# Performance work log

Measured on AMD Instinct MI355X. Metric: run time of the kernel, lower is better.

The kernel has to match this reference:

```python
import jax, jax.numpy as jnp
import numpy as np

W_, H_, D_ = 45, 30, 13
TEXT = 226
NVID = W_ * H_ * D_            # 17550 video tokens
L = TEXT + NVID                # 17776 total tokens
BLK = 128
NKEEP = 32
NBLK = (L + BLK - 1) // BLK    # 139 blocks
LPAD = NBLK * BLK              # 17792
LEVELS = (1, 2, 4, 8)
MASK_RATIOS = ((1, 0.0, 0.05), (2, 0.05, 0.15), (4, 0.15, 0.25), (8, 0.25, 0.5), (0, 0.5, 1.0))
NEG = -1e30

def _sgn(x):
    return (x > 0) - (x < 0)

def _gen3d(x, y, z, ax, ay, az, bx, by, bz, cx, cy, cz):
    w = abs(ax + ay + az); h = abs(bx + by + bz); d = abs(cx + cy + cz)
    dax, day, daz = _sgn(ax), _sgn(ay), _sgn(az)
    dbx, dby, dbz = _sgn(bx), _sgn(by), _sgn(bz)
    dcx, dcy, dcz = _sgn(cx), _sgn(cy), _sgn(cz)
    if h == 1 and d == 1:
        for _ in range(w):
            yield (x, y, z); x += dax; y += day; z += daz
        return
    if w == 1 and d == 1:
        for _ in range(h):
            yield (x, y, z); x += dbx; y += dby; z += dbz
        return
    if w == 1 and h == 1:
        for _ in range(d):
            yield (x, y, z); x += dcx; y += dcy; z += dcz
        return
    ax2, ay2, az2 = ax // 2, ay // 2, az // 2
    bx2, by2, bz2 = bx // 2, by // 2, bz // 2
    cx2, cy2, cz2 = cx // 2, cy // 2, cz // 2
    w2 = abs(ax2 + ay2 + az2); h2 = abs(bx2 + by2 + bz2); d2 = abs(cx2 + cy2 + cz2)
    if (w2 % 2) and (w > 2): ax2 += dax; ay2 += day; az2 += daz
    if (h2 % 2) and (h > 2): bx2 += dbx; by2 += dby; bz2 += dbz
    if (d2 % 2) and (d > 2): cx2 += dcx; cy2 += dcy; cz2 += dcz
    if (2 * w > 3 * h) and (2 * w > 3 * d):
        yield from _gen3d(x, y, z, ax2, ay2, az2, bx, by, bz, cx, cy, cz)
        yield from _gen3d(x + ax2, y + ay2, z + az2, ax - ax2, ay - ay2, az - az2, bx, by, bz, cx, cy, cz)
    elif 3 * h > 4 * d:
        yield from _gen3d(x, y, z, bx2, by2, bz2, cx, cy, cz, ax2, ay2, az2)
        yield from _gen3d(x + bx2, y + by2, z + bz2, ax, ay, az, bx - bx2, by - by2, bz - bz2, cx, cy, cz)
        yield from _gen3d(x + (ax - dax) + (bx2 - dbx), y + (ay - day) + (by2 - dby), z + (az - daz) + (bz2 - dbz), -bx2, -by2, -bz2, cx, cy, cz, -(ax - ax2), -(ay - ay2), -(az - az2))
    elif 3 * d > 4 * h:
        yield from _gen3d(x, y, z, cx2, cy2, cz2, ax2, ay2, az2, bx, by, bz)
        yield from _gen3d(x + cx2, y + cy2, z + cz2, ax, ay, az, bx, by, bz, cx - cx2, cy - cy2, cz - cz2)
        yield from _gen3d(x + (ax - dax) + (cx2 - dcx), y + (ay - day) + (cy2 - dcy), z + (az - daz) + (cz2 - dcz), -cx2, -cy2, -cz2, -(ax - ax2), -(ay - ay2), -(az - az2), bx, by, bz)
    else:
        yield from _gen3d(x, y, z, bx2, by2, bz2, cx2, cy2, cz2, ax2, ay2, az2)
        yield from _gen3d(x + bx2, y + by2, z + bz2, cx, cy, cz, ax2, ay2, az2, bx - bx2, by - by2, bz - bz2)
        yield from _gen3d(x + (bx2 - dbx) + (cx - dcx), y + (by2 - dby) + (cy - dcy), z + (bz2 - dbz) + (cz - dcz), ax, ay, az, -bx2, -by2, -bz2, -(cx - cx2), -(cy - cy2), -(cz - cz2))
        yield from _gen3d(x + (ax - dax) + bx2 + (cx - dcx), y + (ay - day) + by2 + (cy - dcy), z + (az - daz) + bz2 + (cz - dcz), -cx, -cy, -cz, -(ax - ax2), -(ay - ay2), -(az - az2), bx - bx2, by - by2, bz - bz2)

def _gilbert3d(w, h, d):
    if w >= h and w >= d:
        yield from _gen3d(0, 0, 0, w, 0, 0, 0, h, 0, 0, 0, d)
    elif h >= w and h >= d:
        yield from _gen3d(0, 0, 0, 0, h, 0, w, 0, 0, 0, 0, d)
    else:
        yield from _gen3d(0, 0, 0, 0, 0, d, w, 0, 0, 0, h, 0)

def _perms():
    o2g = np.zeros(NVID, np.int64); g2o = np.zeros(NVID, np.int64)
    for g, (x, y, z) in enumerate(_gilbert3d(W_, H_, D_)):
        c = x + W_ * (y + H_ * z)
        o2g[g] = c; g2o[c] = g
    return jnp.asarray(o2g), jnp.asarray(g2o)

O2G, G2O = _perms()

def _sample(x, key):
    # random_sample_tokens: same NKEEP indices (per b,h) reused for every block
    B, Hh, _, Dd = x.shape
    r = jax.random.uniform(key, (B, Hh, BLK))
    idx = jax.lax.top_k(r, NKEEP)[1]                    # [B,H,NKEEP]
    xb = x.reshape(B, Hh, NBLK, BLK, Dd)
    s = jnp.take_along_axis(xb, idx[:, :, None, :, None], axis=3)
    return s.reshape(B, Hh, NBLK * NKEEP, Dd)

def _make_mask(q, k):
    # torch.no_grad() mask path
    q = jax.lax.stop_gradient(q); k = jax.lax.stop_gradient(k)
    pad = LPAD - L
    qp = jnp.pad(q, ((0, 0), (0, 0), (0, pad), (0, 0)), mode='edge')
    kp = jnp.pad(k, ((0, 0), (0, 0), (0, pad), (0, 0)), mode='edge')
    kq, kk = jax.random.split(jax.random.key(0))
    sq = _sample(qp, kq); sk = _sample(kp, kk)
    scale = 1.0 / float(np.sqrt(q.shape[-1]))
    attn = jax.nn.softmax(jnp.einsum('bhid,bhjd->bhij', sq, sk) * scale, axis=-1)
    B, Hh = attn.shape[:2]
    # sum-pool NKEEP x NKEEP -> block-level pooled attention [B,H,NBLK,NBLK]
    pool = attn.reshape(B, Hh, NBLK, NKEEP, NBLK, NKEEP).sum(axis=(3, 5))
    # rank of each column within its row (descending) == scatter over sorted indices
    rank = jnp.argsort(jnp.argsort(-pool, axis=-1), axis=-1)
    mask = jnp.zeros(pool.shape, jnp.int32)
    for val, s, e in MASK_RATIOS:
        si = max(0, int(NBLK * s)); ei = min(NBLK, int(NBLK * e))
        if si < ei and val != 0:
            mask = jnp.where((rank >= si) & (rank < ei), jnp.int32(val), mask)
    mask = mask.at[:, :, :, -2:].set(1)
    mask = mask.at[:, :, -2:, :].set(1)
    return mask

def _pooled_kv(kp, vp):
    # per-level mean-pooled K/V per key block, padded to BLK slots + log-count bias
    B, Hh, _, Dd = kp.shape
    valid = (jnp.arange(LPAD) < L).astype(kp.dtype).reshape(NBLK, BLK)
    kb = kp.reshape(B, Hh, NBLK, BLK, Dd)
    vb = vp.reshape(B, Hh, NBLK, BLK, Dd)
    Ks, Vs, Bs = [], [], []
    for m in LEVELS:
        g = BLK // m
        cnt = valid.reshape(NBLK, g, m).sum(-1)          # [NBLK,g] valid tokens per group
        den = jnp.maximum(cnt, 1.0)
        kpl = kb.reshape(B, Hh, NBLK, g, m, Dd).sum(4) / den[None, None, :, :, None]
        vpl = vb.reshape(B, Hh, NBLK, g, m, Dd).sum(4) / den[None, None, :, :, None]
        bias = jnp.where(cnt > 0, jnp.log(den), NEG)
        padn = BLK - g
        Ks.append(jnp.pad(kpl, ((0, 0), (0, 0), (0, 0), (0, padn), (0, 0))))
        Vs.append(jnp.pad(vpl, ((0, 0), (0, 0), (0, 0), (0, padn), (0, 0))))
        Bs.append(jnp.pad(bias, ((0, 0), (0, padn)), constant_values=NEG))
    return jnp.stack(Ks, 3), jnp.stack(Vs, 3), jnp.stack(Bs, 1)

def _sparse_attn(q, k, v, mask):
    B, Hh, _, Dd = q.shape
    pad = LPAD - L
    zp = ((0, 0), (0, 0), (0, pad), (0, 0))
    qp = jnp.pad(q, zp); kp = jnp.pad(k, zp); vp = jnp.pad(v, zp)
    KL, VL, BIAS = _pooled_kv(kp, vp)   # [B,H,NBLK,4,BLK,D], bias [NBLK,4,BLK]
    table = np.zeros(9, np.int32)
    table[1], table[2], table[4], table[8] = 0, 1, 2, 3
    lvl = jnp.asarray(table)[mask]
    act = mask > 0
    scale = 1.0 / float(np.sqrt(Dd))
    qb = jnp.transpose(qp.reshape(B, Hh, NBLK, BLK, Dd), (2, 0, 1, 3, 4))
    lvl_t = jnp.transpose(lvl, (2, 0, 1, 3))
    act_t = jnp.transpose(act, (2, 0, 1, 3))
    biasB = jnp.broadcast_to(BIAS[None, None], (B, Hh, NBLK, len(LEVELS), BLK))
    def body(carry, xs):
        qi, li, ai = xs                 # [B,H,BLK,D], [B,H,NBLK], [B,H,NBLK]
        sel = li[:, :, :, None, None]
        Ksel = jnp.take_along_axis(KL, sel[..., None], axis=3)[:, :, :, 0]   # [B,H,NBLK,BLK,D]
        Vsel = jnp.take_along_axis(VL, sel[..., None], axis=3)[:, :, :, 0]
        bsel = jnp.take_along_axis(biasB, sel, axis=3)[:, :, :, 0]           # [B,H,NBLK,BLK]
        logit = jnp.einsum('bhqd,bhknd->bhqkn', qi, Ksel) * scale
        logit = logit + jnp.where(ai[:, :, None, :, None], bsel[:, :, None], NEG)
        p = jax.nn.softmax(logit.reshape(B, Hh, BLK, NBLK * BLK), axis=-1)
        o = jnp.einsum('bhqn,bhnd->bhqd', p, Vsel.reshape(B, Hh, NBLK * BLK, Dd))
        return carry, o
    body = jax.checkpoint(body)
    _, outs = jax.lax.scan(body, None, (qb, lvl_t, act_t))
    out = jnp.transpose(outs, (1, 2, 0, 3, 4)).reshape(B, Hh, LPAD, Dd)
    return out[:, :, :L]

def _forward(q, k, v):
    def rearr(x):
        return jnp.concatenate([x[:, :, TEXT:][:, :, O2G], x[:, :, :TEXT]], axis=2)
    qr, kr, vr = rearr(q), rearr(k), rearr(v)
    mask = _make_mask(qr, kr)
    outr = _sparse_attn(qr, kr, vr, mask)
    return jnp.concatenate([outr[:, :, -TEXT:], outr[:, :, :-TEXT][:, :, G2O]], axis=2)

def setup_inputs():
    key = jax.random.key(0)
    kq, kk, kv = jax.random.split(key, 3)
    shp = (1, 8, L, 64)
    return {'q': jax.random.normal(kq, shp, jnp.float32),
            'k': jax.random.normal(kk, shp, jnp.float32),
            'v': jax.random.normal(kv, shp, jnp.float32)}

def reference(q, k, v):
    return _forward(q, k, v)
```

## Files before the change

### kernel.cpp

```cpp
#include <hip/hip_runtime.h>
#include <stdint.h>
#include <string.h>
#include <stdlib.h>

#define JAX_PARTITIONABLE 1

namespace {

constexpr int kW = 45, kH = 30, kD = 13;
constexpr int NVID = kW * kH * kD;
constexpr int TEXT = 226;
constexpr int LSEQ = TEXT + NVID;
constexpr int BLKSZ = 128;
constexpr int NBLK = 139;
constexpr int LPAD = NBLK * BLKSZ;
constexpr int NKEEP = 32;
constexpr int NS = NBLK * NKEEP;
constexpr int NH = 8;
constexpr int DD = 64;
constexpr int VLAST = LSEQ - (NBLK - 1) * BLKSZ;
constexpr float SCALE = 0.125f;
constexpr float SC2 = 0.18033688011120542f;
constexpr float LN2F = 0.69314718055994530942f;
constexpr int MAXG = 188;

constexpr int NGR_H = LPAD / 16;
constexpr int NRAWG = NH * NGR_H;
constexpr int NPOOLG = NH * NBLK * 7;
constexpr int NGALL = NRAWG + NPOOLG;

constexpr int NSPLIT = 16;
constexpr int HCHUNK = (LSEQ + 63) / 64;
constexpr int CHPER = (HCHUNK + NSPLIT - 1) / NSPLIT;
constexpr int NHEAVYB = NH * 2 * NSPLIT;
constexpr int NLIGHT = NH * (NBLK - 2);

constexpr long SZ_RB = (long)NH * LPAD * DD / 2;
constexpr long SZ_SH = (long)NH * NS * DD / 2;
constexpr long SZ_KPB = (long)NH * NBLK * 112 * DD / 2;
constexpr long SZ_KF = (long)NGALL * 1024 / 2;
constexpr long SZ_VF = (long)NGALL * 1024 / 2;
constexpr long SZ_PL = (long)NH * NBLK * NBLK;
constexpr long SZ_O  = (long)NH * LSEQ * DD;
constexpr long SZ_PT = (long)NH * 2 * NSPLIT * BLKSZ * DD;
constexpr long SZ_PS = (long)NH * 2 * NSPLIT * BLKSZ;
constexpr long F_QB = 0;
constexpr long F_KB = F_QB + SZ_RB;
constexpr long F_VB = F_KB + SZ_RB;
constexpr long F_SQH = F_VB + SZ_RB;
constexpr long F_SQM = F_SQH + SZ_SH;
constexpr long F_SQL = F_SQM + SZ_SH;
constexpr long F_SKH = F_SQL + SZ_SH;
constexpr long F_SKM = F_SKH + SZ_SH;
constexpr long F_SKL = F_SKM + SZ_SH;
constexpr long F_KPB = F_SKL + SZ_SH;
constexpr long F_VPB = F_KPB + SZ_KPB;
constexpr long F_KFA = F_VPB + SZ_KPB;
constexpr long F_VFA = F_KFA + SZ_KF;
constexpr long F_PL = F_VFA + SZ_VF;
constexpr long F_MK = F_PL + SZ_PL;
constexpr long F_OR = F_MK + SZ_PL;
constexpr long F_PT = F_OR + SZ_O;
constexpr long F_PS = F_PT + SZ_PT;
constexpr long F_TB = F_PS + SZ_PS;
constexpr int TAB_INTS = 2 * LSEQ + 2 * NH * NKEEP;

struct Gil { int* out; int n; };
static inline int sgn_i(int v) { return (v > 0) - (v < 0); }
static inline int fd2(int a) { return a >= 0 ? a / 2 : -((-a + 1) / 2); }

static void gen3d(Gil& G, int x, int y, int z,
                  int ax, int ay, int az,
                  int bx, int by, int bz,
                  int cx, int cy, int cz) {
  int w = abs(ax + ay + az), h = abs(bx + by + bz), d = abs(cx + cy + cz);
  int dax = sgn_i(ax), day = sgn_i(ay), daz = sgn_i(az);
  int dbx = sgn_i(bx), dby = sgn_i(by), dbz = sgn_i(bz);
  int dcx = sgn_i(cx), dcy = sgn_i(cy), dcz = sgn_i(cz);
  if (h == 1 && d == 1) { for (int i = 0; i < w; i++) { G.out[G.n++] = x + kW * (y + kH * z); x += dax; y += day; z += daz; } return; }
  if (w == 1 && d == 1) { for (int i = 0; i < h; i++) { G.out[G.n++] = x + kW * (y + kH * z); x += dbx; y += dby; z += dbz; } return; }
  if (w == 1 && h == 1) { for (int i = 0; i < d; i++) { G.out[G.n++] = x + kW * (y + kH * z); x += dcx; y += dcy; z += dcz; } return; }
  int ax2 = fd2(ax), ay2 = fd2(ay), az2 = fd2(az);
  int bx2 = fd2(bx), by2 = fd2(by), bz2 = fd2(bz);
  int cx2 = fd2(cx), cy2 = fd2(cy), cz2 = fd2(cz);
  int w2 = abs(ax2 + ay2 + az2), h2 = abs(bx2 + by2 + bz2), d2 = abs(cx2 + cy2 + cz2);
  if ((w2 & 1) && w > 2) { ax2 += dax; ay2 += day; az2 += daz; }
  if ((h2 & 1) && h > 2) { bx2 += dbx; by2 += dby; bz2 += dbz; }
  if ((d2 & 1) && d > 2) { cx2 += dcx; cy2 += dcy; cz2 += dcz; }
  if (2 * w > 3 * h && 2 * w > 3 * d) {
    gen3d(G, x, y, z, ax2, ay2, az2, bx, by, bz, cx, cy, cz);
    gen3d(G, x + ax2, y + ay2, z + az2, ax - ax2, ay - ay2, az - az2, bx, by, bz, cx, cy, cz);
  } else if (3 * h > 4 * d) {
    gen3d(G, x, y, z, bx2, by2, bz2, cx, cy, cz, ax2, ay2, az2);
    gen3d(G, x + bx2, y + by2, z + bz2, ax, ay, az, bx - bx2, by - by2, bz - bz2, cx, cy, cz);
    gen3d(G, x + (ax - dax) + (bx2 - dbx), y + (ay - day) + (by2 - dby), z + (az - daz) + (bz2 - dbz),
          -bx2, -by2, -bz2, cx, cy, cz, -(ax - ax2), -(ay - ay2), -(az - az2));
  } else if (3 * d > 4 * h) {
    gen3d(G, x, y, z, cx2, cy2, cz2, ax2, ay2, az2, bx, by, bz);
    gen3d(G, x + cx2, y + cy2, z + cz2, ax, ay, az, bx, by, bz, cx - cx2, cy - cy2, cz - cz2);
    gen3d(G, x + (ax - dax) + (cx2 - dcx), y + (ay - day) + (cy2 - dcy), z + (az - daz) + (cz2 - dcz),
          -cx2, -cy2, -cz2, -(ax - ax2), -(ay - ay2), -(az - az2), bx, by, bz);
  } else {
    gen3d(G, x, y, z, bx2, by2, bz2, cx2, cy2, cz2, ax2, ay2, az2);
    gen3d(G, x + bx2, y + by2, z + bz2, cx, cy, cz, ax2, ay2, az2, bx - bx2, by - by2, bz - bz2);
    gen3d(G, x + (bx2 - dbx) + (cx - dcx), y + (by2 - dby) + (cy - dcy), z + (bz2 - dbz) + (cz - dcz),
          ax, ay, az, -bx2, -by2, -bz2, -(cx - cx2), -(cy - cy2), -(cz - cz2));
    gen3d(G, x + (ax - dax) + bx2 + (cx - dcx), y + (ay - day) + by2 + (cy - dcy), z + (az - daz) + bz2 + (cz - dcz),
          -cx, -cy, -cz, -(ax - ax2), -(ay - ay2), -(az - az2), bx - bx2, by - by2, bz - bz2);
  }
}

static void tf2x32(uint32_t k0, uint32_t k1, uint32_t x0, uint32_t x1,
                   uint32_t& o0, uint32_t& o1) {
  uint32_t ks0 = k0, ks1 = k1, ks2 = k0 ^ k1 ^ 0x1BD11BDAu;
  const uint32_t ks[3] = {ks0, ks1, ks2};
  const int rot[2][4] = {{13, 15, 26, 6}, {17, 29, 16, 24}};
  x0 += ks[0]; x1 += ks[1];
  for (int i = 0; i < 5; i++) {
    for (int j = 0; j < 4; j++) {
      int rr = rot[i & 1][j];
      x0 += x1;
      x1 = (x1 << rr) | (x1 >> (32 - rr));
      x1 ^= x0;
    }
    x0 += ks[(i + 1) % 3];
    x1 += ks[(i + 2) % 3] + (uint32_t)(i + 1);
  }
  o0 = x0; o1 = x1;
}

static inline float bits_to_unit(uint32_t bits) {
  uint32_t fb = (bits >> 9) | 0x3f800000u;
  float f; memcpy(&f, &fb, 4);
  return f - 1.0f;
}

static void fill_idx(uint32_t K0, uint32_t K1, int* dst) {
  float u[NH * BLKSZ];
#if JAX_PARTITIONABLE
  for (int i = 0; i < NH * BLKSZ; i++) {
    uint32_t a, b; tf2x32(K0, K1, 0u, (uint32_t)i, a, b);
    u[i] = bits_to_unit(a ^ b);
  }
#else
  {
    const int n = NH * BLKSZ, hn = n / 2;
    for (int i = 0; i < hn; i++) {
      uint32_t a, b; tf2x32(K0, K1, (uint32_t)i, (uint32_t)(hn + i), a, b);
      u[i] = bits_to_unit(a);
      u[hn + i] = bits_to_unit(b);
    }
  }
#endif
  for (int h = 0; h < NH; h++) {
    const float* row = u + h * BLKSZ;
    bool used[BLKSZ] = {false};
    for (int r = 0; r < NKEEP; r++) {
      int best = -1; float bv = -2.0f;
      for (int g = 0; g < BLKSZ; g++)
        if (!used[g] && row[g] > bv) { bv = row[g]; best = g; }
      used[best] = true;
      dst[h * NKEEP + r] = best;
    }
  }
}

static void build_tables(int* tab) {
  static int yields[NVID];
  static int o2g_buf[NVID];
  static int g2o_buf[NVID];
  memset(o2g_buf, 0, sizeof(o2g_buf));
  memset(g2o_buf, 0, sizeof(g2o_buf));
  Gil G{yields, 0};
  gen3d(G, 0, 0, 0, kW, 0, 0, 0, kH, 0, 0, 0, kD);
  int n = G.n;
  if (n > NVID) n = NVID;
  for (int g = 0; g < n; g++) o2g_buf[g] = yields[g];
  for (int g = 0; g < n; g++) g2o_buf[yields[g]] = g;

  int* inmap = tab;
  int* outg  = tab + LSEQ;
  for (int g = 0; g < NVID; g++) inmap[g] = TEXT + o2g_buf[g];
  for (int t = 0; t < TEXT; t++) inmap[NVID + t] = t;
  for (int r = 0; r < TEXT; r++) outg[r] = NVID + r;
  for (int c = 0; c < NVID; c++) outg[TEXT + c] = g2o_buf[c];

  uint32_t kq0, kq1, kk0, kk1;
#if JAX_PARTITIONABLE
  tf2x32(0, 0, 0, 0, kq0, kq1);
  tf2x32(0, 0, 0, 1, kk0, kk1);
#else
  {
    uint32_t y00, y10, y01, y11;
    tf2x32(0, 0, 0, 2, y00, y10);
    tf2x32(0, 0, 1, 3, y01, y11);
    kq0 = y00; kq1 = y01; kk0 = y10; kk1 = y11;
  }
#endif
  fill_idx(kq0, kq1, tab + 2 * LSEQ);
  fill_idx(kk0, kk1, tab + 2 * LSEQ + NH * NKEEP);
}

}


typedef __attribute__((ext_vector_type(8))) short short8v;
typedef __attribute__((ext_vector_type(4))) float f32x4;

static __device__ inline unsigned short f2bf(float f) {
  unsigned u = __float_as_uint(f);
  unsigned r = u + 0x7FFFu + ((u >> 16) & 1u);
  return (unsigned short)(r >> 16);
}
static __device__ inline float bf2f(unsigned short s) {
  return __uint_as_float(((unsigned)s) << 16);
}
static __device__ inline int cvtpk(float lo, float hi) {
  int r;
  asm("v_cvt_pk_bf16_f32 %0, %1, %2" : "=v"(r) : "v"(lo), "v"(hi));
  return r;
}

struct KFrag {
  short8v h[2][2], m[2][2], l[2][2];
};
struct KF2 {
  short8v k[4][2];
};


__global__ __launch_bounds__(256) void k_rearr(
    const float* __restrict__ q, const float* __restrict__ k, const float* __restrict__ v,
    short* __restrict__ qrb, short* __restrict__ krb, short* __restrict__ vrb,
    const int* __restrict__ inmap) {
  long gid = (long)blockIdx.x * 256 + threadIdx.x;
  const long totalRows = 3L * NH * LPAD;
  long rowid = gid >> 3;
  int g8 = (int)(gid & 7);
  if (rowid >= totalRows) return;
  int tsel = (int)(rowid / ((long)NH * LPAD));
  long rem = rowid - (long)tsel * NH * LPAD;
  int h = (int)(rem / LPAD);
  int i = (int)(rem % LPAD);
  const float* src = tsel == 0 ? q : (tsel == 1 ? k : v);
  short8v outv;
  if (i < LSEQ) {
    const float* sp = src + ((long)h * LSEQ + inmap[i]) * DD + g8 * 8;
    float4 a = *(const float4*)sp;
    float4 b = *(const float4*)(sp + 4);
    float vals[8] = {a.x, a.y, a.z, a.w, b.x, b.y, b.z, b.w};
#pragma unroll
    for (int j = 0; j < 8; j++) outv[j] = (short)f2bf(vals[j]);
  } else {
#pragma unroll
    for (int j = 0; j < 8; j++) outv[j] = 0;
  }
  short* dst = tsel == 0 ? qrb : (tsel == 1 ? krb : vrb);
  *(short8v*)(dst + ((long)h * LPAD + i) * DD + g8 * 8) = outv;
}

__global__ __launch_bounds__(256) void k_sample(
    const float* __restrict__ q, const float* __restrict__ k,
    short* __restrict__ sqh, short* __restrict__ sqm, short* __restrict__ sql,
    short* __restrict__ skh, short* __restrict__ skm, short* __restrict__ skl,
    const int* __restrict__ qidx, const int* __restrict__ kidx,
    const int* __restrict__ inmap) {
  long gid = (long)blockIdx.x * 256 + threadIdx.x;
  int g = (int)(gid & 7);
  long rowid = gid >> 3;
  const long half = (long)NH * NS;
  if (rowid >= 2 * half) return;
  int tsel = rowid >= half;
  long rem = tsel ? rowid - half : rowid;
  int h = (int)(rem / NS);
  int s = (int)(rem % NS);
  int b = s / NKEEP, t = s % NKEEP;
  const int* idx = tsel ? kidx : qidx;
  int p = b * BLKSZ + idx[h * NKEEP + t];
  if (p >= LSEQ) p = LSEQ - 1;
  int orig = inmap[p];
  const float* src = (tsel ? k : q) + ((long)h * LSEQ + orig) * DD + g * 8;
  float4 a = *(const float4*)src;
  float4 bb = *(const float4*)(src + 4);
  float vals[8] = {a.x, a.y, a.z, a.w, bb.x, bb.y, bb.z, bb.w};
  short8v vh, vm, vl;
#pragma unroll
  for (int j = 0; j < 8; j++) {
    unsigned short hi = f2bf(vals[j]);
    float r1 = vals[j] - bf2f(hi);
    unsigned short mi = f2bf(r1);
    float r2 = r1 - bf2f(mi);
    unsigned short lo = f2bf(r2);
    vh[j] = (short)hi; vm[j] = (short)mi; vl[j] = (short)lo;
  }
  int t16 = s >> 4, lm = s & 15, ks = g >> 2, lg = g & 3;
  long off = (long)h * NS * DD + ((long)(t16 * 2 + ks)) * 512 + (lg * 16 + lm) * 8;
  if (tsel) {
    *(short8v*)(skh + off) = vh;
    *(short8v*)(skm + off) = vm;
    *(short8v*)(skl + off) = vl;
  } else {
    *(short8v*)(sqh + off) = vh;
    *(short8v*)(sqm + off) = vm;
    *(short8v*)(sql + off) = vl;
  }
}

static __device__ inline void ld_frags(
    const short* __restrict__ skh, const short* __restrict__ skm,
    const short* __restrict__ skl, long kbase, int c, int lane, KFrag& F) {
#pragma unroll
  for (int nt = 0; nt < 2; nt++)
#pragma unroll
    for (int ks = 0; ks < 2; ks++) {
      long a = kbase + ((long)((2 * c + nt) * 2 + ks)) * 512 + lane * 8;
      F.h[nt][ks] = *(const short8v*)(skh + a);
      F.m[nt][ks] = *(const short8v*)(skm + a);
      F.l[nt][ks] = *(const short8v*)(skl + a);
    }
}

__global__ __launch_bounds__(256, 2) void k_scores_pool(
    const short* __restrict__ sqh, const short* __restrict__ sqm, const short* __restrict__ sql,
    const short* __restrict__ skh, const short* __restrict__ skm, const short* __restrict__ skl,
    float* __restrict__ pool) {
  __shared__ float bins[32][145];
  __shared__ float invden[32];
  int bid = blockIdx.x;
  int h = bid & 7, qb = bid >> 3;
  int tid = threadIdx.x;
  int wid = tid >> 6, lane = tid & 63;
  int lm = lane & 15, lg = lane >> 4;

  for (int i = tid; i < 32 * 145; i += 256) (&bins[0][0])[i] = 0.f;

  const long base = (long)h * NS * DD;
  short8v Qh[2][2], Qm[2][2], Ql[2][2];
#pragma unroll
  for (int mt = 0; mt < 2; mt++)
#pragma unroll
    for (int ks = 0; ks < 2; ks++) {
      long off = base + ((long)((2 * qb + mt) * 2 + ks)) * 512 + lane * 8;
      Qh[mt][ks] = *(const short8v*)(sqh + off);
      Qm[mt][ks] = *(const short8v*)(sqm + off);
      Ql[mt][ks] = *(const short8v*)(sql + off);
    }
  __syncthreads();

  auto compute = [&](const KFrag& F, int c) {
    f32x4 aq[2][2];
#pragma unroll
    for (int mt = 0; mt < 2; mt++)
#pragma unroll
      for (int nt = 0; nt < 2; nt++) {
        f32x4 a = {0.f, 0.f, 0.f, 0.f};
#pragma unroll
        for (int ks = 0; ks < 2; ks++) {
          a = __builtin_amdgcn_mfma_f32_16x16x32_bf16(F.h[nt][ks], Qh[mt][ks], a, 0, 0, 0);
          a = __builtin_amdgcn_mfma_f32_16x16x32_bf16(F.h[nt][ks], Qm[mt][ks], a, 0, 0, 0);
          a = __builtin_amdgcn_mfma_f32_16x16x32_bf16(F.m[nt][ks], Qh[mt][ks], a, 0, 0, 0);
          a = __builtin_amdgcn_mfma_f32_16x16x32_bf16(F.m[nt][ks], Qm[mt][ks], a, 0, 0, 0);
          a = __builtin_amdgcn_mfma_f32_16x16x32_bf16(F.h[nt][ks], Ql[mt][ks], a, 0, 0, 0);
          a = __builtin_amdgcn_mfma_f32_16x16x32_bf16(F.l[nt][ks], Qh[mt][ks], a, 0, 0, 0);
        }
        aq[mt][nt] = a;
      }
#pragma unroll
    for (int mt = 0; mt < 2; mt++) {
      float s = 0.f;
#pragma unroll
      for (int nt = 0; nt < 2; nt++)
#pragma unroll
        for (int i = 0; i < 4; i++)
          s += __expf(aq[mt][nt][i] * SCALE);
      s += __shfl_xor(s, 16);
      s += __shfl_xor(s, 32);
      if (lg == 0) bins[mt * 16 + lm][c] += s;
    }
  };

  KFrag A, B;
  ld_frags(skh, skm, skl, base, wid, lane, A);
  for (int c = wid; c < NBLK; c += 8) {
    if (c + 4 < NBLK) ld_frags(skh, skm, skl, base, c + 4, lane, B);
    compute(A, c);
    if (c + 4 >= NBLK) break;
    if (c + 8 < NBLK) ld_frags(skh, skm, skl, base, c + 8, lane, A);
    compute(B, c + 4);
  }

  __syncthreads();
  if (tid < 32) {
    float s = 0.f;
    for (int kb = 0; kb < NBLK; kb++) s += bins[tid][kb];
    invden[tid] = 1.0f / s;
  }
  __syncthreads();
  if (tid < NBLK) {
    float s = 0.f;
    for (int r2 = 0; r2 < NKEEP; r2++) s += bins[r2][tid] * invden[r2];
    pool[((long)h * NBLK + qb) * NBLK + tid] = s;
  }
}

__global__ __launch_bounds__(192) void k_mask(
    const float* __restrict__ pool, int* __restrict__ mask) {
  __shared__ float row[NBLK];
  int h = blockIdx.x / NBLK, i = blockIdx.x % NBLK;
  int t = threadIdx.x;
  const float* pr = pool + ((long)h * NBLK + i) * NBLK;
  if (t < NBLK) row[t] = pr[t];
  __syncthreads();
  if (t < NBLK) {
    float pv = row[t];
    int rank = 0;
    for (int j = 0; j < NBLK; j++) {
      float o = row[j];
      rank += (o > pv) || (o == pv && j < t);
    }
    int val = 0;
    if (rank < 6) val = 1;
    else if (rank < 20) val = 2;
    else if (rank < 34) val = 4;
    else if (rank < 69) val = 8;
    if (t >= NBLK - 2) val = 1;
    if (i >= NBLK - 2) val = 1;
    mask[((long)h * NBLK + i) * NBLK + t] = val;
  }
}

__global__ __launch_bounds__(256) void k_poolkv(
    const short* __restrict__ krb, const short* __restrict__ vrb,
    short* __restrict__ Kpb, short* __restrict__ Vpb) {
  long rid = (long)blockIdx.x * 4 + (threadIdx.x >> 6);
  int d = threadIdx.x & 63;
  const long total = 2L * NH * NBLK * 112;
  if (rid >= total) return;
  int tsel = (int)(rid / ((long)NH * NBLK * 112));
  long rem = rid - (long)tsel * NH * NBLK * 112;
  int h = (int)(rem / (NBLK * 112));
  int rem2 = (int)(rem % (NBLK * 112));
  int j = rem2 / 112, p = rem2 % 112;
  int m, g;
  if (p < 64) { m = 2; g = p; }
  else if (p < 96) { m = 4; g = p - 64; }
  else { m = 8; g = p - 96; }
  const short* src = tsel ? vrb : krb;
  const short* base = src + ((long)h * LPAD + j * BLKSZ + g * m) * DD + d;
  float sum = 0.f;
  for (int r2 = 0; r2 < m; r2++) sum += bf2f((unsigned short)base[(long)r2 * DD]);
  short* dst = tsel ? Vpb : Kpb;
  dst[(((long)h * NBLK + j) * 112 + p) * DD + d] = (short)f2bf(sum / (float)m);
}

__global__ __launch_bounds__(256) void k_fragk(
    const short* __restrict__ krb, const short* __restrict__ Kpb,
    short* __restrict__ kfAll) {
  long gid = (long)blockIdx.x * 256 + threadIdx.x;
  if (gid >= (long)NGALL * 128) return;
  int lane = (int)(gid & 63);
  int ks = (int)((gid >> 6) & 1);
  long grp = gid >> 7;
  int lm = lane & 15, lg = lane >> 4;
  const short* srcp;
  long row;
  if (grp < NRAWG) { srcp = krb; row = grp * 16 + lm; }
  else { srcp = Kpb; row = (grp - NRAWG) * 16 + lm; }
  short8v vv = *(const short8v*)(srcp + row * DD + ks * 32 + lg * 8);
  *(short8v*)(kfAll + ((long)grp * 2 + ks) * 512 + lane * 8) = vv;
}

__global__ __launch_bounds__(256) void k_fragv(
    const short* __restrict__ vrb, const short* __restrict__ Vpb,
    short* __restrict__ vfAll) {
  long gid = (long)blockIdx.x * 256 + threadIdx.x;
  if (gid >= (long)NGALL * 256) return;
  int lane = (int)(gid & 63);
  int mtp = (int)((gid >> 6) & 3);
  long grp = gid >> 8;
  int lm = lane & 15, lg = lane >> 4;
  const short* srcp;
  long rowb;
  if (grp < NRAWG) { srcp = vrb; rowb = grp * 16 + lg * 4; }
  else { srcp = Vpb; rowb = (grp - NRAWG) * 16 + lg * 4; }
  short4 o;
  o.x = srcp[(rowb + 0) * DD + mtp * 16 + lm];
  o.y = srcp[(rowb + 1) * DD + mtp * 16 + lm];
  o.z = srcp[(rowb + 2) * DD + mtp * 16 + lm];
  o.w = srcp[(rowb + 3) * DD + mtp * 16 + lm];
  *(short4*)(vfAll + ((long)grp * 4 + mtp) * 256 + lane * 4) = o;
}

__global__ __launch_bounds__(256, 2) void k_attn_light(
    const short* __restrict__ qrb,
    const short* __restrict__ kfAll, const short* __restrict__ vfAll,
    const int* __restrict__ mask,
    float* __restrict__ outr) {
  __shared__ int glist[MAXG];
  __shared__ int ngarr[NBLK];
  __shared__ int wtot[4];
  __shared__ int smeta;

  int bid = blockIdx.x;
  int h = bid / (NBLK - 2);
  int qi = bid % (NBLK - 2);
  int tid = threadIdx.x;
  int lane = tid & 63, wid = tid >> 6;
  int lm = lane & 15, lg = lane >> 4;

  int myng = 0, mylvl = 0, myG = 0;
  if (tid < NBLK) {
    int mv = mask[((long)h * NBLK + qi) * NBLK + tid];
    if (mv) {
      mylvl = (mv == 1) ? 0 : (mv == 2) ? 1 : (mv == 4) ? 2 : 3;
      myG = ((tid == NBLK - 1) ? VLAST : BLKSZ) >> mylvl;
      myng = (myG + 15) >> 4;
    }
  }
  int v = myng;
#pragma unroll
  for (int off = 1; off < 64; off <<= 1) {
    int t2 = __shfl_up(v, off);
    if ((tid & 63) >= off) v += t2;
  }
  if ((tid & 63) == 63) wtot[wid] = v;
  __syncthreads();
  int woff = 0;
#pragma unroll
  for (int w = 0; w < 4; w++) if (w < wid) woff += wtot[w];
  if (tid < NBLK) ngarr[tid] = woff + v - myng;
  if (tid == 0) {
    int tot = wtot[0] + wtot[1] + wtot[2] + wtot[3];
    while (tot & 3) glist[tot++] = 0;
    smeta = tot >> 2;
  }
  __syncthreads();
  if (tid < NBLK && myng) {
    int off = ngarr[tid];
    int grp0;
    if (mylvl == 0) grp0 = h * NGR_H + tid * 8;
    else {
      int l16 = (mylvl == 1) ? 0 : (mylvl == 2) ? 4 : 6;
      grp0 = NRAWG + (h * NBLK + tid) * 7 + l16;
    }
    for (int g = 0; g < myng; g++) {
      int cnt = myG - 16 * g; if (cnt > 16) cnt = 16;
      glist[off + g] = (grp0 + g) | (cnt << 24) | (mylvl << 29);
    }
  }
  __syncthreads();
  int nchunks = smeta;

  short8v Qf[2][2];
#pragma unroll
  for (int mt = 0; mt < 2; mt++)
#pragma unroll
    for (int ks = 0; ks < 2; ks++) {
      long row = (long)h * LPAD + qi * BLKSZ + wid * 32 + mt * 16 + lm;
      Qf[mt][ks] = *(const short8v*)(qrb + row * DD + ks * 32 + lg * 8);
    }

  f32x4 Oacc[4][2];
#pragma unroll
  for (int a = 0; a < 4; a++)
#pragma unroll
    for (int b = 0; b < 2; b++) { f32x4 z = {0.f, 0.f, 0.f, 0.f}; Oacc[a][b] = z; }
  float lrow0 = 0.f, lrow1 = 0.f;

  auto ldK = [&](int c, KF2& F) {
#pragma unroll
    for (int g = 0; g < 4; g++) {
      long grp = (long)((unsigned)glist[4 * c + g] & 0xFFFFFFu);
#pragma unroll
      for (int ks = 0; ks < 2; ks++)
        F.k[g][ks] = *(const short8v*)(kfAll + (grp * 2 + ks) * 512 + lane * 8);
    }
  };

  auto doChunk = [&](const KF2& F, int c) {
    int cntv[4]; float biasv[4]; long grpv[4];
#pragma unroll
    for (int g = 0; g < 4; g++) {
      unsigned e = (unsigned)glist[4 * c + g];
      grpv[g] = (long)(e & 0xFFFFFFu);
      cntv[g] = (e >> 24) & 31;
      biasv[g] = (float)((e >> 29) & 3);
    }
    short4 Vfr[4][4];
#pragma unroll
    for (int g = 0; g < 4; g++)
#pragma unroll
      for (int mtp = 0; mtp < 4; mtp++)
        Vfr[g][mtp] = *(const short4*)(vfAll + (grpv[g] * 4 + mtp) * 256 + lane * 4);
    bool allfull = (cntv[0] == 16) & (cntv[1] == 16) & (cntv[2] == 16) & (cntv[3] == 16);

    short8v Pf[2][2];
#pragma unroll
    for (int mt = 0; mt < 2; mt++) {
      f32x4 aq[4];
#pragma unroll
      for (int nt = 0; nt < 4; nt++) {
        f32x4 z = {0.f, 0.f, 0.f, 0.f};
        f32x4 a = __builtin_amdgcn_mfma_f32_16x16x32_bf16(F.k[nt][0], Qf[mt][0], z, 0, 0, 0);
        aq[nt] = __builtin_amdgcn_mfma_f32_16x16x32_bf16(F.k[nt][1], Qf[mt][1], a, 0, 0, 0);
      }
      float ps[16];
      if (allfull) {
#pragma unroll
        for (int nt = 0; nt < 4; nt++)
#pragma unroll
          for (int i = 0; i < 4; i++)
            ps[nt * 4 + i] = exp2f(fmaf(aq[nt][i], SC2, biasv[nt]));
      } else {
#pragma unroll
        for (int nt = 0; nt < 4; nt++)
#pragma unroll
          for (int i = 0; i < 4; i++) {
            int kvr = lg * 4 + i;
            ps[nt * 4 + i] = (kvr < cntv[nt]) ? exp2f(fmaf(aq[nt][i], SC2, biasv[nt])) : 0.f;
          }
      }
      float lsum = 0.f;
#pragma unroll
      for (int i = 0; i < 16; i++) lsum += ps[i];
      if (mt == 0) lrow0 += lsum; else lrow1 += lsum;
#pragma unroll
      for (int H = 0; H < 2; H++) {
        union { int i[4]; short8v v; } u;
        u.i[0] = cvtpk(ps[8 * H + 0], ps[8 * H + 1]);
        u.i[1] = cvtpk(ps[8 * H + 2], ps[8 * H + 3]);
        u.i[2] = cvtpk(ps[8 * H + 4], ps[8 * H + 5]);
        u.i[3] = cvtpk(ps[8 * H + 6], ps[8 * H + 7]);
        Pf[mt][H] = u.v;
      }
    }
#pragma unroll
    for (int mtp = 0; mtp < 4; mtp++)
#pragma unroll
      for (int H = 0; H < 2; H++) {
        short4 lo = Vfr[2 * H][mtp], hi = Vfr[2 * H + 1][mtp];
        short8v vf;
        vf[0] = lo.x; vf[1] = lo.y; vf[2] = lo.z; vf[3] = lo.w;
        vf[4] = hi.x; vf[5] = hi.y; vf[6] = hi.z; vf[7] = hi.w;
        Oacc[mtp][0] = __builtin_amdgcn_mfma_f32_16x16x32_bf16(vf, Pf[0][H], Oacc[mtp][0], 0, 0, 0);
        Oacc[mtp][1] = __builtin_amdgcn_mfma_f32_16x16x32_bf16(vf, Pf[1][H], Oacc[mtp][1], 0, 0, 0);
      }
  };

  KF2 A, B;
  ldK(0, A);
  for (int c = 0; c < nchunks; c += 2) {
    if (c + 1 < nchunks) ldK(c + 1, B);
    doChunk(A, c);
    if (c + 1 >= nchunks) break;
    if (c + 2 < nchunks) ldK(c + 2, A);
    doChunk(B, c + 1);
  }

  lrow0 += __shfl_xor(lrow0, 16); lrow0 += __shfl_xor(lrow0, 32);
  lrow1 += __shfl_xor(lrow1, 16); lrow1 += __shfl_xor(lrow1, 32);
  float inv0 = 1.0f / lrow0, inv1 = 1.0f / lrow1;
#pragma unroll
  for (int mt = 0; mt < 2; mt++) {
    int grow = qi * BLKSZ + wid * 32 + mt * 16 + lm;
    float inv = mt ? inv1 : inv0;
    float* orow = outr + ((long)h * LSEQ + grow) * DD;
#pragma unroll
    for (int mtp = 0; mtp < 4; mtp++) {
      f32x4 o = Oacc[mtp][mt];
      *(float4*)(orow + mtp * 16 + lg * 4) =
          make_float4(o[0] * inv, o[1] * inv, o[2] * inv, o[3] * inv);
    }
  }
}

__global__ __launch_bounds__(256, 1) void k_attn_heavy(
    const short* __restrict__ qrb, const short* __restrict__ krb,
    const short* __restrict__ vrb,
    float* __restrict__ part, float* __restrict__ plsum) {
  __shared__ __align__(16) short Kt[64 * 64];
  __shared__ __align__(16) short Vt[64 * 68];

  int bid = blockIdx.x;
  int split = bid & (NSPLIT - 1);
  int hq = bid / NSPLIT;
  int h = hq >> 1;
  int qi = NBLK - 2 + (hq & 1);
  int c0 = split * CHPER;
  int c1 = c0 + CHPER; if (c1 > HCHUNK) c1 = HCHUNK;
  int slot = hq * NSPLIT + split;
  int tid = threadIdx.x;

  int lane = tid & 63, wid = tid >> 6;
  int lm = lane & 15, lg = lane >> 4;

  short8v Qf[2][2];
#pragma unroll
  for (int mt = 0; mt < 2; mt++)
#pragma unroll
    for (int ks = 0; ks < 2; ks++) {
      long row = (long)h * LPAD + qi * BLKSZ + wid * 32 + mt * 16 + lm;
      Qf[mt][ks] = *(const short8v*)(qrb + row * DD + ks * 32 + lg * 8);
    }

  f32x4 Oacc[4][2];
#pragma unroll
  for (int a = 0; a < 4; a++)
#pragma unroll
    for (int b = 0; b < 2; b++) { f32x4 z = {0.f, 0.f, 0.f, 0.f}; Oacc[a][b] = z; }
  float lrow0 = 0.f, lrow1 = 0.f;

  int sr = tid & 63;
  int sd0 = (tid >> 6) * 16;

  short8v pkA, pkB, pvA, pvB;
  {
    long src = (long)h * LPAD + (long)c0 * 64 + sr;
    const short8v* kp = (const short8v*)(krb + src * DD + sd0);
    const short8v* vp = (const short8v*)(vrb + src * DD + sd0);
    pkA = kp[0]; pkB = kp[1];
    pvA = vp[0]; pvB = vp[1];
  }

  for (int c = c0; c < c1; c++) {
    __syncthreads();
    {
      int sw = (sr & 7) << 3;
      *(short8v*)&Kt[sr * 64 + (sd0 ^ sw)] = pkA;
      *(short8v*)&Kt[sr * 64 + ((sd0 + 8) ^ sw)] = pkB;
#pragma unroll
      for (int i = 0; i < 8; i++) {
        Vt[(sd0 + i) * 68 + sr] = pvA[i];
        Vt[(sd0 + 8 + i) * 68 + sr] = pvB[i];
      }
    }
    __syncthreads();
    if (c + 1 < c1) {
      long src = (long)h * LPAD + (long)(c + 1) * 64 + sr;
      const short8v* kp = (const short8v*)(krb + src * DD + sd0);
      const short8v* vp = (const short8v*)(vrb + src * DD + sd0);
      pkA = kp[0]; pkB = kp[1];
      pvA = vp[0]; pvB = vp[1];
    }

    bool allfull = (c != HCHUNK - 1);

    short8v Kf[4][2];
#pragma unroll
    for (int nt = 0; nt < 4; nt++)
#pragma unroll
      for (int ks = 0; ks < 2; ks++)
        Kf[nt][ks] = *(short8v*)&Kt[(nt * 16 + lm) * 64 + ((ks * 32 + lg * 8) ^ ((lm & 7) << 3))];

    short8v Pf[2][2];
#pragma unroll
    for (int mt = 0; mt < 2; mt++) {
      f32x4 aq[4];
#pragma unroll
      for (int nt = 0; nt < 4; nt++) {
        f32x4 z = {0.f, 0.f, 0.f, 0.f};
        f32x4 a = __builtin_amdgcn_mfma_f32_16x16x32_bf16(Kf[nt][0], Qf[mt][0], z, 0, 0, 0);
        aq[nt] = __builtin_amdgcn_mfma_f32_16x16x32_bf16(Kf[nt][1], Qf[mt][1], a, 0, 0, 0);
      }
      float ps[16];
      if (allfull) {
#pragma unroll
        for (int nt = 0; nt < 4; nt++)
#pragma unroll
          for (int i = 0; i < 4; i++)
            ps[nt * 4 + i] = __expf(aq[nt][i] * SCALE);
      } else {
#pragma unroll
        for (int nt = 0; nt < 4; nt++) {
          int cc = LSEQ - 16 * (4 * c + nt);
          int cnt = cc <= 0 ? 0 : (cc >= 16 ? 16 : cc);
#pragma unroll
          for (int i = 0; i < 4; i++) {
            int kvr = lg * 4 + i;
            ps[nt * 4 + i] = (kvr < cnt) ? __expf(aq[nt][i] * SCALE) : 0.f;
          }
        }
      }
      float lsum = 0.f;
#pragma unroll
      for (int i = 0; i < 16; i++) lsum += ps[i];
      if (mt == 0) lrow0 += lsum; else lrow1 += lsum;
#pragma unroll
      for (int H = 0; H < 2; H++) {
        union { int i[4]; short8v v; } u;
        u.i[0] = cvtpk(ps[8 * H + 0], ps[8 * H + 1]);
        u.i[1] = cvtpk(ps[8 * H + 2], ps[8 * H + 3]);
        u.i[2] = cvtpk(ps[8 * H + 4], ps[8 * H + 5]);
        u.i[3] = cvtpk(ps[8 * H + 6], ps[8 * H + 7]);
        Pf[mt][H] = u.v;
      }
    }

#pragma unroll
    for (int mtp = 0; mtp < 4; mtp++) {
      int d68 = (mtp * 16 + lm) * 68;
#pragma unroll
      for (int H = 0; H < 2; H++) {
        short4 lo = *(short4*)&Vt[d68 + H * 32 + lg * 4];
        short4 hi = *(short4*)&Vt[d68 + H * 32 + 16 + lg * 4];
        short8v vf;
        vf[0] = lo.x; vf[1] = lo.y; vf[2] = lo.z; vf[3] = lo.w;
        vf[4] = hi.x; vf[5] = hi.y; vf[6] = hi.z; vf[7] = hi.w;
        Oacc[mtp][0] = __builtin_amdgcn_mfma_f32_16x16x32_bf16(vf, Pf[0][H], Oacc[mtp][0], 0, 0, 0);
        Oacc[mtp][1] = __builtin_amdgcn_mfma_f32_16x16x32_bf16(vf, Pf[1][H], Oacc[mtp][1], 0, 0, 0);
      }
    }
  }

  lrow0 += __shfl_xor(lrow0, 16); lrow0 += __shfl_xor(lrow0, 32);
  lrow1 += __shfl_xor(lrow1, 16); lrow1 += __shfl_xor(lrow1, 32);
  if (lg == 0) {
    plsum[(long)slot * BLKSZ + wid * 32 + lm] = lrow0;
    plsum[(long)slot * BLKSZ + wid * 32 + 16 + lm] = lrow1;
  }
#pragma unroll
  for (int mt = 0; mt < 2; mt++) {
    int lrow = wid * 32 + mt * 16 + lm;
    float* orow = part + ((long)slot * BLKSZ + lrow) * DD;
#pragma unroll
    for (int mtp = 0; mtp < 4; mtp++) {
      f32x4 o = Oacc[mtp][mt];
      *(float4*)(orow + mtp * 16 + lg * 4) = make_float4(o[0], o[1], o[2], o[3]);
    }
  }
}

__global__ __launch_bounds__(256) void k_combine(
    const float* __restrict__ part, const float* __restrict__ plsum,
    float* __restrict__ outr) {
  int hq = blockIdx.x;
  int h = hq >> 1;
  int qi = NBLK - 2 + (hq & 1);
  int t = threadIdx.x;
  int row = t >> 1;
  int dbase = (t & 1) * 32;
  float l = 0.f;
  for (int s = 0; s < NSPLIT; s++) l += plsum[(long)(hq * NSPLIT + s) * BLKSZ + row];
  int grow = qi * BLKSZ + row;
  if (grow >= LSEQ) return;
  float inv = 1.0f / l;
  float* orow = outr + ((long)h * LSEQ + grow) * DD;
  for (int d = dbase; d < dbase + 32; d += 4) {
    float4 acc = make_float4(0.f, 0.f, 0.f, 0.f);
    for (int s = 0; s < NSPLIT; s++) {
      float4 p4 = *(const float4*)&part[((long)(hq * NSPLIT + s) * BLKSZ + row) * DD + d];
      acc.x += p4.x; acc.y += p4.y; acc.z += p4.z; acc.w += p4.w;
    }
    *(float4*)(orow + d) = make_float4(acc.x * inv, acc.y * inv, acc.z * inv, acc.w * inv);
  }
}

__global__ __launch_bounds__(256) void k_out(
    const float* __restrict__ outr, const int* __restrict__ outg,
    float* __restrict__ out) {
  long rid = (long)blockIdx.x * 4 + (threadIdx.x >> 6);
  int d = threadIdx.x & 63;
  const long total = (long)NH * LSEQ;
  if (rid >= total) return;
  int h = (int)(rid / LSEQ);
  int r = (int)(rid % LSEQ);
  int src = outg[r];
  out[((long)h * LSEQ + r) * DD + d] = outr[((long)h * LSEQ + src) * DD + d];
}


extern "C" void kernel_launch(void* const* d_in, const int* in_sizes, int n_in,
                              void* d_out, int out_size, void* d_ws, size_t ws_size,
                              hipStream_t stream) {
  (void)in_sizes; (void)n_in; (void)out_size; (void)ws_size;
  const float* q = (const float*)d_in[0];
  const float* k = (const float*)d_in[1];
  const float* v = (const float*)d_in[2];
  float* ws = (float*)d_ws;
  float* out = (float*)d_out;

  static int* htab = nullptr;
  if (!htab) { (void)hipHostMalloc((void**)&htab, TAB_INTS * sizeof(int)); }
  build_tables(htab);

  int* dtab = (int*)(ws + F_TB);
  int* inmap = dtab;
  int* outg = dtab + LSEQ;
  int* qidx = dtab + 2 * LSEQ;
  int* kidx = qidx + NH * NKEEP;
  int* dmask = (int*)(ws + F_MK);
  short* qrb = (short*)(ws + F_QB);
  short* krb = (short*)(ws + F_KB);
  short* vrb = (short*)(ws + F_VB);
  short* sqh = (short*)(ws + F_SQH);
  short* sqm = (short*)(ws + F_SQM);
  short* sql = (short*)(ws + F_SQL);
  short* skh = (short*)(ws + F_SKH);
  short* skm = (short*)(ws + F_SKM);
  short* skl = (short*)(ws + F_SKL);
  short* Kpb = (short*)(ws + F_KPB);
  short* Vpb = (short*)(ws + F_VPB);
  short* kfAll = (short*)(ws + F_KFA);
  short* vfAll = (short*)(ws + F_VFA);
  float* pool = ws + F_PL;
  float* outr = ws + F_OR;
  float* part = ws + F_PT;
  float* plsum = ws + F_PS;

  hipMemcpyAsync(dtab, htab, TAB_INTS * sizeof(int), hipMemcpyHostToDevice, stream);

  {
    long thr = 3L * NH * LPAD * 8;
    k_rearr<<<dim3((unsigned)((thr + 255) / 256)), 256, 0, stream>>>(
        q, k, v, qrb, krb, vrb, inmap);
  }
  {
    long thr = 2L * NH * NS * 8;
    k_sample<<<dim3((unsigned)((thr + 255) / 256)), 256, 0, stream>>>(
        q, k, sqh, sqm, sql, skh, skm, skl, qidx, kidx, inmap);
  }
  k_scores_pool<<<dim3(NH * NBLK), 256, 0, stream>>>(
      sqh, sqm, sql, skh, skm, skl, pool);
  k_mask<<<dim3(NH * NBLK), 192, 0, stream>>>(pool, dmask);
  {
    long rows = 2L * NH * NBLK * 112;
    k_poolkv<<<dim3((unsigned)((rows + 3) / 4)), 256, 0, stream>>>(krb, vrb, Kpb, Vpb);
  }
  {
    long thr = (long)NGALL * 128;
    k_fragk<<<dim3((unsigned)((thr + 255) / 256)), 256, 0, stream>>>(krb, Kpb, kfAll);
  }
  {
    long thr = (long)NGALL * 256;
    k_fragv<<<dim3((unsigned)((thr + 255) / 256)), 256, 0, stream>>>(vrb, Vpb, vfAll);
  }
  k_attn_heavy<<<dim3(NHEAVYB), 256, 0, stream>>>(qrb, krb, vrb, part, plsum);
  k_attn_light<<<dim3(NLIGHT), 256, 0, stream>>>(qrb, kfAll, vfAll, dmask, outr);
  k_combine<<<dim3(NH * 2), 256, 0, stream>>>(part, plsum, outr);
  {
    long rows = (long)NH * LSEQ;
    k_out<<<dim3((unsigned)((rows + 3) / 4)), 256, 0, stream>>>(outr, outg, out);
  }
}
```

Baseline: 509.6 us.

## Stage K/V fragments in LDS and split light attention blocks into halves

The light attention kernel now launches twice as many blocks, each covering 64 query rows (16 per wave) instead of 128. K and V fragments for each chunk are loaded once per block cooperatively into shared memory with a register-prefetch stage, then read by all four waves. Previously each wave loaded them from global memory itself. This cuts redundant global loads and per-wave register pressure. In exchange it adds two barriers per chunk, and the per-block mask and group-list setup is duplicated across both halves.

Result: faster. 491.0 us (-3.7%).

```diff
diff --git a/kernel.cpp b/kernel.cpp
--- a/kernel.cpp
+++ b/kernel.cpp
@@ -21,7 +21,6 @@
 constexpr int VLAST = LSEQ - (NBLK - 1) * BLKSZ;
 constexpr float SCALE = 0.125f;
 constexpr float SC2 = 0.18033688011120542f;
-constexpr float LN2F = 0.69314718055994530942f;
 constexpr int MAXG = 188;
 
 constexpr int NGR_H = LPAD / 16;
@@ -33,7 +32,7 @@
 constexpr int HCHUNK = (LSEQ + 63) / 64;
 constexpr int CHPER = (HCHUNK + NSPLIT - 1) / NSPLIT;
 constexpr int NHEAVYB = NH * 2 * NSPLIT;
-constexpr int NLIGHT = NH * (NBLK - 2);
+constexpr int NLIGHT2 = NH * (NBLK - 2) * 2;
 
 constexpr long SZ_RB = (long)NH * LPAD * DD / 2;
 constexpr long SZ_SH = (long)NH * NS * DD / 2;
@@ -224,9 +223,6 @@
 struct KFrag {
   short8v h[2][2], m[2][2], l[2][2];
 };
-struct KF2 {
-  short8v k[4][2];
-};
 
 
 __global__ __launch_bounds__(256) void k_rearr(
@@ -497,13 +493,16 @@
     const int* __restrict__ mask,
     float* __restrict__ outr) {
   __shared__ int glist[MAXG];
-  __shared__ int ngarr[NBLK];
   __shared__ int wtot[4];
   __shared__ int smeta;
+  __shared__ __align__(16) short KtF[4096];
+  __shared__ __align__(16) short VtF[4096];
 
   int bid = blockIdx.x;
-  int h = bid / (NBLK - 2);
-  int qi = bid % (NBLK - 2);
+  int half = bid & 1;
+  int lb = bid >> 1;
+  int h = lb / (NBLK - 2);
+  int qi = lb % (NBLK - 2);
   int tid = threadIdx.x;
   int lane = tid & 63, wid = tid >> 6;
   int lm = lane & 15, lg = lane >> 4;
@@ -528,7 +527,7 @@
   int woff = 0;
 #pragma unroll
   for (int w = 0; w < 4; w++) if (w < wid) woff += wtot[w];
-  if (tid < NBLK) ngarr[tid] = woff + v - myng;
+  int myoff = woff + v - myng;
   if (tid == 0) {
     int tot = wtot[0] + wtot[1] + wtot[2] + wtot[3];
     while (tot & 3) glist[tot++] = 0;
@@ -536,7 +535,6 @@
   }
   __syncthreads();
   if (tid < NBLK && myng) {
-    int off = ngarr[tid];
     int grp0;
     if (mylvl == 0) grp0 = h * NGR_H + tid * 8;
     else {
@@ -545,129 +543,129 @@
     }
     for (int g = 0; g < myng; g++) {
       int cnt = myG - 16 * g; if (cnt > 16) cnt = 16;
-      glist[off + g] = (grp0 + g) | (cnt << 24) | (mylvl << 29);
+      glist[myoff + g] = (grp0 + g) | (cnt << 24) | (mylvl << 29);
     }
   }
   __syncthreads();
   int nchunks = smeta;
 
-  short8v Qf[2][2];
-#pragma unroll
-  for (int mt = 0; mt < 2; mt++)
-#pragma unroll
-    for (int ks = 0; ks < 2; ks++) {
-      long row = (long)h * LPAD + qi * BLKSZ + wid * 32 + mt * 16 + lm;
-      Qf[mt][ks] = *(const short8v*)(qrb + row * DD + ks * 32 + lg * 8);
-    }
-
-  f32x4 Oacc[4][2];
-#pragma unroll
-  for (int a = 0; a < 4; a++)
-#pragma unroll
-    for (int b = 0; b < 2; b++) { f32x4 z = {0.f, 0.f, 0.f, 0.f}; Oacc[a][b] = z; }
-  float lrow0 = 0.f, lrow1 = 0.f;
-
-  auto ldK = [&](int c, KF2& F) {
-#pragma unroll
-    for (int g = 0; g < 4; g++) {
-      long grp = (long)((unsigned)glist[4 * c + g] & 0xFFFFFFu);
-#pragma unroll
-      for (int ks = 0; ks < 2; ks++)
-        F.k[g][ks] = *(const short8v*)(kfAll + (grp * 2 + ks) * 512 + lane * 8);
+  short8v Qf[2];
+  {
+    long row = (long)h * LPAD + qi * BLKSZ + half * 64 + wid * 16 + lm;
+    Qf[0] = *(const short8v*)(qrb + row * DD + lg * 8);
+    Qf[1] = *(const short8v*)(qrb + row * DD + 32 + lg * 8);
+  }
+  f32x4 Oacc[4];
+#pragma unroll
+  for (int a = 0; a < 4; a++) { f32x4 z = {0.f, 0.f, 0.f, 0.f}; Oacc[a] = z; }
+  float lrow = 0.f;
+
+  short8v rk0, rk1, rv0, rv1;
+  auto ldStage = [&](int c) {
+    {
+      int s = tid;
+      long grp = (long)((unsigned)glist[4 * c + (s >> 7)] & 0xFFFFFFu);
+      rk0 = *(const short8v*)(kfAll + (grp * 2 + ((s >> 6) & 1)) * 512 + (long)(s & 63) * 8);
+      s = tid + 256;
+      grp = (long)((unsigned)glist[4 * c + (s >> 7)] & 0xFFFFFFu);
+      rk1 = *(const short8v*)(kfAll + (grp * 2 + ((s >> 6) & 1)) * 512 + (long)(s & 63) * 8);
+    }
+    {
+      int s = tid;
+      long grp = (long)((unsigned)glist[4 * c + (s >> 7)] & 0xFFFFFFu);
+      rv0 = *(const short8v*)(vfAll + (grp * 4 + ((s >> 5) & 3)) * 256 + (long)(s & 31) * 8);
+      s = tid + 256;
+      grp = (long)((unsigned)glist[4 * c + (s >> 7)] & 0xFFFFFFu);
+      rv1 = *(const short8v*)(vfAll + (grp * 4 + ((s >> 5) & 3)) * 256 + (long)(s & 31) * 8);
     }
   };
-
-  auto doChunk = [&](const KF2& F, int c) {
-    int cntv[4]; float biasv[4]; long grpv[4];
+  auto stStage = [&]() {
+    *(short8v*)&KtF[tid * 8] = rk0;
+    *(short8v*)&KtF[(tid + 256) * 8] = rk1;
+    {
+      int s = tid;
+      int g = s >> 7, mtp = (s >> 5) & 3, l = s & 31;
+      int base = (mtp * 2 + (g >> 1)) * 512 + ((g & 1) * 4) + l * 16;
+      *(short4*)&VtF[base] = make_short4(rv0[0], rv0[1], rv0[2], rv0[3]);
+      *(short4*)&VtF[base + 8] = make_short4(rv0[4], rv0[5], rv0[6], rv0[7]);
+      s = tid + 256;
+      g = s >> 7; mtp = (s >> 5) & 3; l = s & 31;
+      base = (mtp * 2 + (g >> 1)) * 512 + ((g & 1) * 4) + l * 16;
+      *(short4*)&VtF[base] = make_short4(rv1[0], rv1[1], rv1[2], rv1[3]);
+      *(short4*)&VtF[base + 8] = make_short4(rv1[4], rv1[5], rv1[6], rv1[7]);
+    }
+  };
+
+  ldStage(0);
+  for (int c = 0; c < nchunks; c++) {
+    __syncthreads();
+    stStage();
+    __syncthreads();
+    if (c + 1 < nchunks) ldStage(c + 1);
+
+    int cntv[4]; float biasv[4];
 #pragma unroll
     for (int g = 0; g < 4; g++) {
       unsigned e = (unsigned)glist[4 * c + g];
-      grpv[g] = (long)(e & 0xFFFFFFu);
       cntv[g] = (e >> 24) & 31;
       biasv[g] = (float)((e >> 29) & 3);
     }
-    short4 Vfr[4][4];
-#pragma unroll
-    for (int g = 0; g < 4; g++)
-#pragma unroll
-      for (int mtp = 0; mtp < 4; mtp++)
-        Vfr[g][mtp] = *(const short4*)(vfAll + (grpv[g] * 4 + mtp) * 256 + lane * 4);
     bool allfull = (cntv[0] == 16) & (cntv[1] == 16) & (cntv[2] == 16) & (cntv[3] == 16);
 
-    short8v Pf[2][2];
-#pragma unroll
-    for (int mt = 0; mt < 2; mt++) {
-      f32x4 aq[4];
-#pragma unroll
-      for (int nt = 0; nt < 4; nt++) {
-        f32x4 z = {0.f, 0.f, 0.f, 0.f};
-        f32x4 a = __builtin_amdgcn_mfma_f32_16x16x32_bf16(F.k[nt][0], Qf[mt][0], z, 0, 0, 0);
-        aq[nt] = __builtin_amdgcn_mfma_f32_16x16x32_bf16(F.k[nt][1], Qf[mt][1], a, 0, 0, 0);
-      }
-      float ps[16];
-      if (allfull) {
-#pragma unroll
-        for (int nt = 0; nt < 4; nt++)
-#pragma unroll
-          for (int i = 0; i < 4; i++)
-            ps[nt * 4 + i] = exp2f(fmaf(aq[nt][i], SC2, biasv[nt]));
-      } else {
-#pragma unroll
-        for (int nt = 0; nt < 4; nt++)
-#pragma unroll
-          for (int i = 0; i < 4; i++) {
-            int kvr = lg * 4 + i;
-            ps[nt * 4 + i] = (kvr < cntv[nt]) ? exp2f(fmaf(aq[nt][i], SC2, biasv[nt])) : 0.f;
-          }
-      }
-      float lsum = 0.f;
-#pragma unroll
-      for (int i = 0; i < 16; i++) lsum += ps[i];
-      if (mt == 0) lrow0 += lsum; else lrow1 += lsum;
-#pragma unroll
-      for (int H = 0; H < 2; H++) {
-        union { int i[4]; short8v v; } u;
-        u.i[0] = cvtpk(ps[8 * H + 0], ps[8 * H + 1]);
-        u.i[1] = cvtpk(ps[8 * H + 2], ps[8 * H + 3]);
-        u.i[2] = cvtpk(ps[8 * H + 4], ps[8 * H + 5]);
-        u.i[3] = cvtpk(ps[8 * H + 6], ps[8 * H + 7]);
-        Pf[mt][H] = u.v;
-      }
-    }
-#pragma unroll
-    for (int mtp = 0; mtp < 4; mtp++)
-#pragma unroll
-      for (int H = 0; H < 2; H++) {
-        short4 lo = Vfr[2 * H][mtp], hi = Vfr[2 * H + 1][mtp];
-        short8v vf;
-        vf[0] = lo.x; vf[1] = lo.y; vf[2] = lo.z; vf[3] = lo.w;
-        vf[4] = hi.x; vf[5] = hi.y; vf[6] = hi.z; vf[7] = hi.w;
-        Oacc[mtp][0] = __builtin_amdgcn_mfma_f32_16x16x32_bf16(vf, Pf[0][H], Oacc[mtp][0], 0, 0, 0);
-        Oacc[mtp][1] = __builtin_amdgcn_mfma_f32_16x16x32_bf16(vf, Pf[1][H], Oacc[mtp][1], 0, 0, 0);
-      }
-  };
-
-  KF2 A, B;
-  ldK(0, A);
-  for (int c = 0; c < nchunks; c += 2) {
-    if (c + 1 < nchunks) ldK(c + 1, B);
-    doChunk(A, c);
-    if (c + 1 >= nchunks) break;
-    if (c + 2 < nchunks) ldK(c + 2, A);
-    doChunk(B, c + 1);
-  }
-
-  lrow0 += __shfl_xor(lrow0, 16); lrow0 += __shfl_xor(lrow0, 32);
-  lrow1 += __shfl_xor(lrow1, 16); lrow1 += __shfl_xor(lrow1, 32);
-  float inv0 = 1.0f / lrow0, inv1 = 1.0f / lrow1;
-#pragma unroll
-  for (int mt = 0; mt < 2; mt++) {
-    int grow = qi * BLKSZ + wid * 32 + mt * 16 + lm;
-    float inv = mt ? inv1 : inv0;
+    f32x4 aq[4];
+#pragma unroll
+    for (int nt = 0; nt < 4; nt++) {
+      short8v k0 = *(short8v*)&KtF[(nt * 2 + 0) * 512 * 2 / 2 + lane * 8];
+      short8v k1 = *(short8v*)&KtF[(nt * 2 + 1) * 512 + lane * 8];
+      f32x4 z = {0.f, 0.f, 0.f, 0.f};
+      f32x4 a = __builtin_amdgcn_mfma_f32_16x16x32_bf16(k0, Qf[0], z, 0, 0, 0);
+      aq[nt] = __builtin_amdgcn_mfma_f32_16x16x32_bf16(k1, Qf[1], a, 0, 0, 0);
+    }
+    float ps[16];
+    if (allfull) {
+#pragma unroll
+      for (int nt = 0; nt < 4; nt++)
+#pragma unroll
+        for (int i = 0; i < 4; i++)
+          ps[nt * 4 + i] = exp2f(fmaf(aq[nt][i], SC2, biasv[nt]));
+    } else {
+#pragma unroll
+      for (int nt = 0; nt < 4; nt++)
+#pragma unroll
+        for (int i = 0; i < 4; i++) {
+          int kvr = lg * 4 + i;
+          ps[nt * 4 + i] = (kvr < cntv[nt]) ? exp2f(fmaf(aq[nt][i], SC2, biasv[nt])) : 0.f;
+        }
+    }
+#pragma unroll
+    for (int i = 0; i < 16; i++) lrow += ps[i];
+    short8v Pf[2];
+#pragma unroll
+    for (int H = 0; H < 2; H++) {
+      union { int i[4]; short8v v; } u;
+      u.i[0] = cvtpk(ps[8 * H + 0], ps[8 * H + 1]);
+      u.i[1] = cvtpk(ps[8 * H + 2], ps[8 * H + 3]);
+      u.i[2] = cvtpk(ps[8 * H + 4], ps[8 * H + 5]);
+      u.i[3] = cvtpk(ps[8 * H + 6], ps[8 * H + 7]);
+      Pf[H] = u.v;
+    }
+#pragma unroll
+    for (int mtp = 0; mtp < 4; mtp++) {
+      short8v vf0 = *(short8v*)&VtF[(mtp * 2 + 0) * 512 + lane * 8];
+      short8v vf1 = *(short8v*)&VtF[(mtp * 2 + 1) * 512 + lane * 8];
+      Oacc[mtp] = __builtin_amdgcn_mfma_f32_16x16x32_bf16(vf0, Pf[0], Oacc[mtp], 0, 0, 0);
+      Oacc[mtp] = __builtin_amdgcn_mfma_f32_16x16x32_bf16(vf1, Pf[1], Oacc[mtp], 0, 0, 0);
+    }
+  }
+
+  lrow += __shfl_xor(lrow, 16); lrow += __shfl_xor(lrow, 32);
+  float inv = 1.0f / lrow;
+  {
+    int grow = qi * BLKSZ + half * 64 + wid * 16 + lm;
     float* orow = outr + ((long)h * LSEQ + grow) * DD;
 #pragma unroll
     for (int mtp = 0; mtp < 4; mtp++) {
-      f32x4 o = Oacc[mtp][mt];
+      f32x4 o = Oacc[mtp];
       *(float4*)(orow + mtp * 16 + lg * 4) =
           make_float4(o[0] * inv, o[1] * inv, o[2] * inv, o[3] * inv);
     }
@@ -935,7 +933,7 @@
     k_fragv<<<dim3((unsigned)((thr + 255) / 256)), 256, 0, stream>>>(vrb, Vpb, vfAll);
   }
   k_attn_heavy<<<dim3(NHEAVYB), 256, 0, stream>>>(qrb, krb, vrb, part, plsum);
-  k_attn_light<<<dim3(NLIGHT), 256, 0, stream>>>(qrb, kfAll, vfAll, dmask, outr);
+  k_attn_light<<<dim3(NLIGHT2), 256, 0, stream>>>(qrb, kfAll, vfAll, dmask, outr);
   k_combine<<<dim3(NH * 2), 256, 0, stream>>>(part, plsum, outr);
   {
     long rows = (long)NH * LSEQ;
```
